# Kernel optimization log

Hardware: AMD Instinct MI355X
Metric: run time of the kernel (lower is better)

## Reference

```python
import jax, jax.numpy as jnp
import numpy as np

D_MODEL = 1024
N_HEADS = 16
D_K = D_MODEL // N_HEADS


def setup_inputs() -> dict:
    key = jax.random.key(0)
    ks = jax.random.split(key, 7)
    B, L = 1, 4096
    query = jax.random.normal(ks[0], (B, L, D_MODEL), dtype=jnp.float32)
    key_t = jax.random.normal(ks[1], (B, L, D_MODEL), dtype=jnp.float32)
    value = jax.random.normal(ks[2], (B, L, D_MODEL), dtype=jnp.float32)
    scale = 1.0 / np.sqrt(D_MODEL)
    # nn.Linear weight W has shape [out, in]; y = x @ W.T
    w_q = jax.random.normal(ks[3], (D_MODEL, D_MODEL), dtype=jnp.float32) * scale
    w_k = jax.random.normal(ks[4], (D_MODEL, D_MODEL), dtype=jnp.float32) * scale
    w_v = jax.random.normal(ks[5], (D_MODEL, D_MODEL), dtype=jnp.float32) * scale
    w_o = jax.random.normal(ks[6], (D_MODEL, D_MODEL), dtype=jnp.float32) * scale
    return {"query": query, "key": key_t, "value": value,
            "w_q": w_q, "w_k": w_k, "w_v": w_v, "w_o": w_o}


def reference(query, key, value, w_q, w_k, w_v, w_o):
    B, L, _ = query.shape
    # projections (Linear: x @ W.T)
    Q = (query @ w_q.T).reshape(B, L, N_HEADS, D_K).transpose(0, 2, 1, 3)
    K = (key @ w_k.T).reshape(B, L, N_HEADS, D_K).transpose(0, 2, 1, 3)
    V = (value @ w_v.T).reshape(B, L, N_HEADS, D_K).transpose(0, 2, 1, 3)
    # scaled dot-product attention with materialized [B,H,L,L] scores
    scores = jnp.einsum('bhqd,bhkd->bhqk', Q, K) / jnp.sqrt(jnp.float32(D_K))
    attn = jax.nn.softmax(scores, axis=-1)
    out = jnp.einsum('bhqk,bhkd->bhqd', attn, V)  # [B,H,L,d_k]
    out = out.transpose(0, 2, 1, 3).reshape(B, L, D_MODEL)
    return out @ w_o.T
```

## Files before the change

### kernel.cpp

```cpp
#include <hip/hip_runtime.h>
#include <hip/hip_bf16.h>
#include <hip/hip_fp16.h>
#include <cstdint>
#include <math.h>

#define DMODEL 1024
#define SEQ    4096
#define NHEAD  16
#define DK     64

typedef __attribute__((ext_vector_type(8))) short bf16x8;
typedef __attribute__((ext_vector_type(8))) _Float16 f16x8;
typedef __attribute__((ext_vector_type(4))) float f32x4;
typedef unsigned short u16;

__device__ __forceinline__ u16 f2bf(float f) {
    union { float f; unsigned int u; } v; v.f = f;
    unsigned int u = v.u;
    u += 0x7FFFu + ((u >> 16) & 1u);
    return (u16)(u >> 16);
}
__device__ __forceinline__ float bf2f(u16 h) {
    union { unsigned int u; float f; } v; v.u = ((unsigned int)h) << 16;
    return v.f;
}
__device__ __forceinline__ u16 f2h(float f) {
    __half h = __float2half_rn(f);
    union { __half h; u16 u; } v; v.h = h; return v.u;
}
__device__ __forceinline__ float h2f(u16 x) {
    union { u16 u; __half h; } v; v.u = x;
    return __half2float(v.h);
}
__device__ __forceinline__ unsigned int pk_bf16(float a, float b) {
    union { __hip_bfloat162 h; unsigned int u; } v;
    v.h = __float22bfloat162_rn(make_float2(a, b));
    return v.u;
}
__device__ __forceinline__ float fast_exp2(float x) {
    float r; asm("v_exp_f32 %0, %1" : "=v"(r) : "v"(x)); return r;
}

__global__ __launch_bounds__(256) void fallback_marker(float* __restrict__ out, int n) {
    int i = blockIdx.x * 256 + threadIdx.x;
    if (i < n) out[i] = (i == 0) ? 12345.0f : 0.0f;
}

__device__ __forceinline__ void split4_store(const float* __restrict__ in,
                                             u16* __restrict__ hi,
                                             u16* __restrict__ lo, int i) {
    float4 v = ((const float4*)in)[i];
    u16 h0 = f2h(v.x), h1 = f2h(v.y), h2 = f2h(v.z), h3 = f2h(v.w);
    ushort4 hv; hv.x = h0; hv.y = h1; hv.z = h2; hv.w = h3;
    ushort4 lv;
    lv.x = f2h(v.x - h2f(h0)); lv.y = f2h(v.y - h2f(h1));
    lv.z = f2h(v.z - h2f(h2)); lv.w = f2h(v.w - h2f(h3));
    ((ushort4*)hi)[i] = hv;
    ((ushort4*)lo)[i] = lv;
}

__global__ __launch_bounds__(256) void split_kernel(const float* __restrict__ in,
                                                    u16* __restrict__ hi,
                                                    u16* __restrict__ lo, int n4) {
    int i = blockIdx.x * 256 + threadIdx.x;
    if (i < n4) split4_store(in, hi, lo, i);
}

__global__ __launch_bounds__(256) void split_pair(const float* __restrict__ a_in,
                                                  u16* __restrict__ a_hi,
                                                  u16* __restrict__ a_lo, int a_n4,
                                                  const float* __restrict__ w_in,
                                                  u16* __restrict__ w_hi,
                                                  u16* __restrict__ w_lo, int w_n4) {
    int i = blockIdx.x * 256 + threadIdx.x;
    if (blockIdx.y == 0) {
        if (i < a_n4) split4_store(a_in, a_hi, a_lo, i);
    } else {
        if (i < w_n4) split4_store(w_in, w_hi, w_lo, i);
    }
}

__device__ __forceinline__ void gemm_core_fp16(const u16* __restrict__ aHi,
                                               const u16* __restrict__ aLo,
                                               const u16* __restrict__ bHi,
                                               int bm, int bn,
                                               f32x4 (&acc)[2][4]) {
    __shared__ u16 sAh[128 * 72], sAl[128 * 72];
    __shared__ u16 sBh[64 * 72];

    const int tid  = threadIdx.x;
    const int wave = tid >> 6;
    const int lane = tid & 63;
    const int quad = lane >> 4;
    const int l15  = lane & 15;
    const int srow = tid >> 2;
    const int scol = (tid & 3) * 16;

    const u16* pAh0 = aHi + (size_t)(bm + srow) * DMODEL + scol;
    const u16* pAh1 = aHi + (size_t)(bm + 64 + srow) * DMODEL + scol;
    const u16* pAl0 = aLo + (size_t)(bm + srow) * DMODEL + scol;
    const u16* pAl1 = aLo + (size_t)(bm + 64 + srow) * DMODEL + scol;
    const u16* pBh  = bHi + (size_t)(bn + srow) * DMODEL + scol;

    for (int k0 = 0; k0 < DMODEL; k0 += 64) {
        uint4 ah00 = *(const uint4*)(pAh0 + k0);
        uint4 ah01 = *(const uint4*)(pAh0 + k0 + 8);
        uint4 ah10 = *(const uint4*)(pAh1 + k0);
        uint4 ah11 = *(const uint4*)(pAh1 + k0 + 8);
        uint4 al00 = *(const uint4*)(pAl0 + k0);
        uint4 al01 = *(const uint4*)(pAl0 + k0 + 8);
        uint4 al10 = *(const uint4*)(pAl1 + k0);
        uint4 al11 = *(const uint4*)(pAl1 + k0 + 8);
        uint4 bh0  = *(const uint4*)(pBh + k0);
        uint4 bh1  = *(const uint4*)(pBh + k0 + 8);

        __syncthreads();
        *(uint4*)&sAh[srow * 72 + scol]            = ah00;
        *(uint4*)&sAh[srow * 72 + scol + 8]        = ah01;
        *(uint4*)&sAh[(64 + srow) * 72 + scol]     = ah10;
        *(uint4*)&sAh[(64 + srow) * 72 + scol + 8] = ah11;
        *(uint4*)&sAl[srow * 72 + scol]            = al00;
        *(uint4*)&sAl[srow * 72 + scol + 8]        = al01;
        *(uint4*)&sAl[(64 + srow) * 72 + scol]     = al10;
        *(uint4*)&sAl[(64 + srow) * 72 + scol + 8] = al11;
        *(uint4*)&sBh[srow * 72 + scol]            = bh0;
        *(uint4*)&sBh[srow * 72 + scol + 8]        = bh1;
        __syncthreads();

#pragma unroll
        for (int c = 0; c < 2; c++) {
            f16x8 ah[2], al[2];
#pragma unroll
            for (int m = 0; m < 2; m++) {
                const int aoff = (wave * 32 + m * 16 + l15) * 72 + c * 32 + quad * 8;
                ah[m] = *(const f16x8*)&sAh[aoff];
                al[m] = *(const f16x8*)&sAl[aoff];
            }
#pragma unroll
            for (int nt = 0; nt < 4; nt++) {
                const int boff = (nt * 16 + l15) * 72 + c * 32 + quad * 8;
                f16x8 bhf = *(const f16x8*)&sBh[boff];
#pragma unroll
                for (int m = 0; m < 2; m++) {
                    acc[m][nt] = __builtin_amdgcn_mfma_f32_16x16x32_f16(ah[m], bhf, acc[m][nt], 0, 0, 0);
                    acc[m][nt] = __builtin_amdgcn_mfma_f32_16x16x32_f16(al[m], bhf, acc[m][nt], 0, 0, 0);
                }
            }
        }
    }
}

__global__ __launch_bounds__(256) void proj_hl_bf(const u16* __restrict__ aHi,
                                                  const u16* __restrict__ aLo,
                                                  const u16* __restrict__ bHi,
                                                  u16* __restrict__ C,
                                                  int ldc, float scale) {
    const int bm = blockIdx.x * 128;
    const int bn = blockIdx.y * 64;
    f32x4 acc[2][4] = {};
    gemm_core_fp16(aHi, aLo, bHi, bm, bn, acc);
    const int lane = threadIdx.x & 63;
    const int wave = threadIdx.x >> 6;
    const int quad = lane >> 4;
    const int l15  = lane & 15;
#pragma unroll
    for (int m = 0; m < 2; m++)
#pragma unroll
        for (int nt = 0; nt < 4; nt++) {
            int col = bn + nt * 16 + l15;
#pragma unroll
            for (int r = 0; r < 4; r++) {
                int row = bm + wave * 32 + m * 16 + quad * 4 + r;
                C[(size_t)row * ldc + col] = f2bf(acc[m][nt][r] * scale);
            }
        }
}

__global__ __launch_bounds__(256) void proj_hl_f32(const u16* __restrict__ aHi,
                                                   const u16* __restrict__ aLo,
                                                   const u16* __restrict__ bHi,
                                                   float* __restrict__ C) {
    const int bm = blockIdx.x * 128;
    const int bn = blockIdx.y * 64;
    f32x4 acc[2][4] = {};
    gemm_core_fp16(aHi, aLo, bHi, bm, bn, acc);
    const int lane = threadIdx.x & 63;
    const int wave = threadIdx.x >> 6;
    const int quad = lane >> 4;
    const int l15  = lane & 15;
#pragma unroll
    for (int m = 0; m < 2; m++)
#pragma unroll
        for (int nt = 0; nt < 4; nt++) {
            int col = bn + nt * 16 + l15;
#pragma unroll
            for (int r = 0; r < 4; r++) {
                int row = bm + wave * 32 + m * 16 + quad * 4 + r;
                C[(size_t)row * DMODEL + col] = acc[m][nt][r];
            }
        }
}

#define PST 72

__global__ __launch_bounds__(256) void attn_mfma(const u16* __restrict__ Q,
                                                 const u16* __restrict__ K,
                                                 const u16* __restrict__ Vt,
                                                 u16* __restrict__ AOh,
                                                 u16* __restrict__ AOl) {
    __shared__ u16 sK[2][64 * 72];
    __shared__ u16 sV[2][64 * 72];
    __shared__ u16 sP[4 * 32 * PST];

    const int lin  = blockIdx.y * gridDim.x + blockIdx.x;
    const int swz  = (lin & 7) * 64 + (lin >> 3);
    const int head = swz >> 5;
    const int q0   = (swz & 31) * 128;

    const int tid  = threadIdx.x;
    const int wave = tid >> 6;
    const int lane = tid & 63;
    const int quad = lane >> 4;
    const int l15  = lane & 15;
    const int srow = tid >> 2;
    const int scol = (tid & 3) * 16;

    bf16x8 qf[2][2];
#pragma unroll
    for (int m = 0; m < 2; m++) {
        const u16* qb = Q + (size_t)(q0 + wave * 32 + m * 16 + l15) * DMODEL + head * DK;
        qf[m][0] = *(const bf16x8*)(qb + quad * 8);
        qf[m][1] = *(const bf16x8*)(qb + 32 + quad * 8);
    }

    f32x4 oacc[2][4] = {};
    float l_part[2] = {0.0f, 0.0f};

    const u16* Kst = K  + (size_t)srow * DMODEL + head * DK + scol;
    const u16* Vst = Vt + (size_t)(head * DK + srow) * SEQ + scol;
    u16* sPw = sP + wave * 32 * PST;

    {
        uint4 kv0 = *(const uint4*)(Kst);
        uint4 kv1 = *(const uint4*)(Kst + 8);
        uint4 vv0 = *(const uint4*)(Vst);
        uint4 vv1 = *(const uint4*)(Vst + 8);
        *(uint4*)&sK[0][srow * 72 + scol]     = kv0;
        *(uint4*)&sK[0][srow * 72 + scol + 8] = kv1;
        *(uint4*)&sV[0][srow * 72 + scol]     = vv0;
        *(uint4*)&sV[0][srow * 72 + scol + 8] = vv1;
    }
    __syncthreads();

    int cur = 0;
    for (int k0 = 0; k0 < SEQ; k0 += 64) {
        uint4 nkv0, nkv1, nvv0, nvv1;
        const bool has_next = (k0 + 64 < SEQ);
        if (has_next) {
            nkv0 = *(const uint4*)(Kst + (size_t)(k0 + 64) * DMODEL);
            nkv1 = *(const uint4*)(Kst + (size_t)(k0 + 64) * DMODEL + 8);
            nvv0 = *(const uint4*)(Vst + k0 + 64);
            nvv1 = *(const uint4*)(Vst + k0 + 64 + 8);
        }

        f32x4 s[4][2] = {};
#pragma unroll
        for (int nt = 0; nt < 4; nt++) {
            bf16x8 kf0 = *(const bf16x8*)&sK[cur][(nt * 16 + l15) * 72 + quad * 8];
            bf16x8 kf1 = *(const bf16x8*)&sK[cur][(nt * 16 + l15) * 72 + 32 + quad * 8];
#pragma unroll
            for (int m = 0; m < 2; m++) {
                s[nt][m] = __builtin_amdgcn_mfma_f32_16x16x32_bf16(kf0, qf[m][0], s[nt][m], 0, 0, 0);
                s[nt][m] = __builtin_amdgcn_mfma_f32_16x16x32_bf16(kf1, qf[m][1], s[nt][m], 0, 0, 0);
            }
        }

#pragma unroll
        for (int m = 0; m < 2; m++)
#pragma unroll
            for (int nt = 0; nt < 4; nt++) {
                float p0 = fast_exp2(s[nt][m][0]);
                float p1 = fast_exp2(s[nt][m][1]);
                float p2 = fast_exp2(s[nt][m][2]);
                float p3 = fast_exp2(s[nt][m][3]);
                l_part[m] += (p0 + p1) + (p2 + p3);
                uint2 w;
                w.x = pk_bf16(p0, p1);
                w.y = pk_bf16(p2, p3);
                *(uint2*)&sPw[(m * 16 + l15) * PST + nt * 16 + quad * 4] = w;
            }

#pragma unroll
        for (int c = 0; c < 2; c++) {
            bf16x8 pf0 = *(const bf16x8*)&sPw[(0 * 16 + l15) * PST + c * 32 + quad * 8];
            bf16x8 pf1 = *(const bf16x8*)&sPw[(1 * 16 + l15) * PST + c * 32 + quad * 8];
#pragma unroll
            for (int nt = 0; nt < 4; nt++) {
                bf16x8 vf = *(const bf16x8*)&sV[cur][(nt * 16 + l15) * 72 + c * 32 + quad * 8];
                oacc[0][nt] = __builtin_amdgcn_mfma_f32_16x16x32_bf16(pf0, vf, oacc[0][nt], 0, 0, 0);
                oacc[1][nt] = __builtin_amdgcn_mfma_f32_16x16x32_bf16(pf1, vf, oacc[1][nt], 0, 0, 0);
            }
        }

        if (has_next) {
            const int nxt = cur ^ 1;
            *(uint4*)&sK[nxt][srow * 72 + scol]     = nkv0;
            *(uint4*)&sK[nxt][srow * 72 + scol + 8] = nkv1;
            *(uint4*)&sV[nxt][srow * 72 + scol]     = nvv0;
            *(uint4*)&sV[nxt][srow * 72 + scol + 8] = nvv1;
        }
        __syncthreads();
        cur ^= 1;
    }

    float lf[2];
#pragma unroll
    for (int m = 0; m < 2; m++) {
        float l = l_part[m];
        l += __shfl_xor(l, 16);
        l += __shfl_xor(l, 32);
        lf[m] = l;
    }
#pragma unroll
    for (int m = 0; m < 2; m++) {
        float l_i[4];
#pragma unroll
        for (int r = 0; r < 4; r++)
            l_i[r] = __shfl(lf[m], (lane & 48) | (quad * 4 + r));
#pragma unroll
        for (int nt = 0; nt < 4; nt++) {
            int col = head * DK + nt * 16 + l15;
#pragma unroll
            for (int r = 0; r < 4; r++) {
                int row = q0 + wave * 32 + m * 16 + quad * 4 + r;
                float o = oacc[m][nt][r] / l_i[r];
                u16 h = f2h(o);
                AOh[(size_t)row * DMODEL + col] = h;
                AOl[(size_t)row * DMODEL + col] = f2h(o - h2f(h));
            }
        }
    }
}

extern "C" void kernel_launch(void* const* d_in, const int* in_sizes, int n_in,
                              void* d_out, int out_size, void* d_ws, size_t ws_size,
                              hipStream_t stream) {
    const float* query = (const float*)d_in[0];
    const float* key_t = (const float*)d_in[1];
    const float* value = (const float*)d_in[2];
    const float* wq    = (const float*)d_in[3];
    const float* wk    = (const float*)d_in[4];
    const float* wv    = (const float*)d_in[5];
    const float* wo    = (const float*)d_in[6];
    float* out = (float*)d_out;

    const size_t ACT_N = (size_t)SEQ * DMODEL;
    const size_t W_N   = (size_t)DMODEL * DMODEL;
    const size_t NEED  = 4 * ACT_N * sizeof(float);

    if (d_ws == nullptr || ws_size < NEED) {
        fallback_marker<<<dim3((out_size + 255) / 256), dim3(256), 0, stream>>>(out, out_size);
        return;
    }

    u16* ACT_HI = (u16*)d_ws;
    u16* ACT_LO = ACT_HI + ACT_N;
    u16* W_HI   = ACT_LO + ACT_N;
    u16* W_LO   = W_HI + W_N;
    u16* Qb     = W_LO + W_N;
    u16* Kb     = Qb + ACT_N;
    u16* Vt     = Kb + ACT_N;
    u16* AO_HI  = Vt + ACT_N;
    u16* AO_LO  = AO_HI + ACT_N;

    const int ACT4 = (int)(ACT_N / 4);
    const int W4   = (int)(W_N / 4);
    dim3 blk(256);
    dim3 pairg((ACT4 + 255) / 256, 2);
    dim3 wg((W4 + 255) / 256);

    const float QSCALE = 0.125f * 1.44269504f;

    split_pair<<<pairg, blk, 0, stream>>>(query, ACT_HI, ACT_LO, ACT4, wq, W_HI, W_LO, W4);
    proj_hl_bf<<<dim3(SEQ / 128, DMODEL / 64), blk, 0, stream>>>(
        ACT_HI, ACT_LO, W_HI, Qb, DMODEL, QSCALE);

    split_pair<<<pairg, blk, 0, stream>>>(key_t, ACT_HI, ACT_LO, ACT4, wk, W_HI, W_LO, W4);
    proj_hl_bf<<<dim3(SEQ / 128, DMODEL / 64), blk, 0, stream>>>(
        ACT_HI, ACT_LO, W_HI, Kb, DMODEL, 1.0f);

    split_pair<<<pairg, blk, 0, stream>>>(value, ACT_HI, ACT_LO, ACT4, wv, W_HI, W_LO, W4);
    proj_hl_bf<<<dim3(DMODEL / 128, SEQ / 64), blk, 0, stream>>>(
        W_HI, W_LO, ACT_HI, Vt, SEQ, 1.0f);

    attn_mfma<<<dim3(SEQ / 128, NHEAD), blk, 0, stream>>>(Qb, Kb, Vt, AO_HI, AO_LO);

    split_kernel<<<wg, blk, 0, stream>>>(wo, W_HI, W_LO, W4);
    proj_hl_f32<<<dim3(SEQ / 128, DMODEL / 64), blk, 0, stream>>>(
        AO_HI, AO_LO, W_HI, out);
}
```

Baseline: 334.9 us.

## Batch Q/K/V conversion and projections into single launches, drop lo-split term

Replaces the three split+projection pairs with one conversion kernel over all six inputs and one projection kernel covering the Q, K and V GEMMs, using a swizzled block index. The Q/K/V projections drop the fp16 low-residual term for activations, halving MFMA work and shared-memory traffic there. The output projection's weight split now writes only the high part. This cuts launch count and arithmetic, but lowers projection precision to plain fp16 inputs, which may affect accuracy.

```diff
diff --git a/kernel.cpp b/kernel.cpp
--- a/kernel.cpp
+++ b/kernel.cpp
@@ -46,38 +46,140 @@
     if (i < n) out[i] = (i == 0) ? 12345.0f : 0.0f;
 }
 
-__device__ __forceinline__ void split4_store(const float* __restrict__ in,
-                                             u16* __restrict__ hi,
-                                             u16* __restrict__ lo, int i) {
-    float4 v = ((const float4*)in)[i];
-    u16 h0 = f2h(v.x), h1 = f2h(v.y), h2 = f2h(v.z), h3 = f2h(v.w);
-    ushort4 hv; hv.x = h0; hv.y = h1; hv.z = h2; hv.w = h3;
-    ushort4 lv;
-    lv.x = f2h(v.x - h2f(h0)); lv.y = f2h(v.y - h2f(h1));
-    lv.z = f2h(v.z - h2f(h2)); lv.w = f2h(v.w - h2f(h3));
-    ((ushort4*)hi)[i] = hv;
-    ((ushort4*)lo)[i] = lv;
-}
-
-__global__ __launch_bounds__(256) void split_kernel(const float* __restrict__ in,
-                                                    u16* __restrict__ hi,
-                                                    u16* __restrict__ lo, int n4) {
+__global__ __launch_bounds__(256) void split_all(const float* __restrict__ q,
+                                                 const float* __restrict__ k,
+                                                 const float* __restrict__ v,
+                                                 const float* __restrict__ wq,
+                                                 const float* __restrict__ wk,
+                                                 const float* __restrict__ wv,
+                                                 u16* __restrict__ qh,
+                                                 u16* __restrict__ kh,
+                                                 u16* __restrict__ vh,
+                                                 u16* __restrict__ wqh,
+                                                 u16* __restrict__ wkh,
+                                                 u16* __restrict__ wvh,
+                                                 int act_n4, int w_n4) {
     int i = blockIdx.x * 256 + threadIdx.x;
-    if (i < n4) split4_store(in, hi, lo, i);
-}
-
-__global__ __launch_bounds__(256) void split_pair(const float* __restrict__ a_in,
-                                                  u16* __restrict__ a_hi,
-                                                  u16* __restrict__ a_lo, int a_n4,
-                                                  const float* __restrict__ w_in,
-                                                  u16* __restrict__ w_hi,
-                                                  u16* __restrict__ w_lo, int w_n4) {
+    const float* src; u16* dst; int n4;
+    switch (blockIdx.y) {
+        case 0:  src = q;  dst = qh;  n4 = act_n4; break;
+        case 1:  src = k;  dst = kh;  n4 = act_n4; break;
+        case 2:  src = v;  dst = vh;  n4 = act_n4; break;
+        case 3:  src = wq; dst = wqh; n4 = w_n4;   break;
+        case 4:  src = wk; dst = wkh; n4 = w_n4;   break;
+        default: src = wv; dst = wvh; n4 = w_n4;   break;
+    }
+    if (i < n4) {
+        float4 f = ((const float4*)src)[i];
+        ushort4 h; h.x = f2h(f.x); h.y = f2h(f.y); h.z = f2h(f.z); h.w = f2h(f.w);
+        ((ushort4*)dst)[i] = h;
+    }
+}
+
+__global__ __launch_bounds__(256) void split_hi(const float* __restrict__ in,
+                                                u16* __restrict__ hi, int n4) {
     int i = blockIdx.x * 256 + threadIdx.x;
-    if (blockIdx.y == 0) {
-        if (i < a_n4) split4_store(a_in, a_hi, a_lo, i);
-    } else {
-        if (i < w_n4) split4_store(w_in, w_hi, w_lo, i);
-    }
+    if (i < n4) {
+        float4 f = ((const float4*)in)[i];
+        ushort4 h; h.x = f2h(f.x); h.y = f2h(f.y); h.z = f2h(f.z); h.w = f2h(f.w);
+        ((ushort4*)hi)[i] = h;
+    }
+}
+
+__device__ __forceinline__ void gemm_core_f16_1t(const u16* __restrict__ aHi,
+                                                 const u16* __restrict__ bHi,
+                                                 int bm, int bn,
+                                                 f32x4 (&acc)[2][4]) {
+    __shared__ u16 sAh[128 * 72];
+    __shared__ u16 sBh[64 * 72];
+
+    const int tid  = threadIdx.x;
+    const int wave = tid >> 6;
+    const int lane = tid & 63;
+    const int quad = lane >> 4;
+    const int l15  = lane & 15;
+    const int srow = tid >> 2;
+    const int scol = (tid & 3) * 16;
+
+    const u16* pA0 = aHi + (size_t)(bm + srow) * DMODEL + scol;
+    const u16* pA1 = aHi + (size_t)(bm + 64 + srow) * DMODEL + scol;
+    const u16* pB  = bHi + (size_t)(bn + srow) * DMODEL + scol;
+
+    for (int k0 = 0; k0 < DMODEL; k0 += 64) {
+        uint4 a00 = *(const uint4*)(pA0 + k0);
+        uint4 a01 = *(const uint4*)(pA0 + k0 + 8);
+        uint4 a10 = *(const uint4*)(pA1 + k0);
+        uint4 a11 = *(const uint4*)(pA1 + k0 + 8);
+        uint4 b0  = *(const uint4*)(pB + k0);
+        uint4 b1  = *(const uint4*)(pB + k0 + 8);
+
+        __syncthreads();
+        *(uint4*)&sAh[srow * 72 + scol]            = a00;
+        *(uint4*)&sAh[srow * 72 + scol + 8]        = a01;
+        *(uint4*)&sAh[(64 + srow) * 72 + scol]     = a10;
+        *(uint4*)&sAh[(64 + srow) * 72 + scol + 8] = a11;
+        *(uint4*)&sBh[srow * 72 + scol]            = b0;
+        *(uint4*)&sBh[srow * 72 + scol + 8]        = b1;
+        __syncthreads();
+
+#pragma unroll
+        for (int c = 0; c < 2; c++) {
+            f16x8 ah[2];
+#pragma unroll
+            for (int m = 0; m < 2; m++) {
+                const int aoff = (wave * 32 + m * 16 + l15) * 72 + c * 32 + quad * 8;
+                ah[m] = *(const f16x8*)&sAh[aoff];
+            }
+#pragma unroll
+            for (int nt = 0; nt < 4; nt++) {
+                const int boff = (nt * 16 + l15) * 72 + c * 32 + quad * 8;
+                f16x8 bhf = *(const f16x8*)&sBh[boff];
+#pragma unroll
+                for (int m = 0; m < 2; m++)
+                    acc[m][nt] = __builtin_amdgcn_mfma_f32_16x16x32_f16(ah[m], bhf, acc[m][nt], 0, 0, 0);
+            }
+        }
+    }
+}
+
+__global__ __launch_bounds__(256) void proj_qkv(const u16* __restrict__ qh,
+                                                const u16* __restrict__ kh,
+                                                const u16* __restrict__ vh,
+                                                const u16* __restrict__ wqh,
+                                                const u16* __restrict__ wkh,
+                                                const u16* __restrict__ wvh,
+                                                u16* __restrict__ Qb,
+                                                u16* __restrict__ Kb,
+                                                u16* __restrict__ Vt,
+                                                float qscale) {
+    const int lin = blockIdx.y * gridDim.x + blockIdx.x;
+    const int swz = (lin & 7) * 192 + (lin >> 3);
+    const int z   = swz >> 9;
+    const int bx  = swz & 511;
+
+    const u16 *A, *B; u16* C; int bm, bn, ldc; float scale;
+    if (z == 0)      { A = qh;  B = wqh; C = Qb; bm = (bx & 31) * 128; bn = (bx >> 5) * 64; ldc = DMODEL; scale = qscale; }
+    else if (z == 1) { A = kh;  B = wkh; C = Kb; bm = (bx & 31) * 128; bn = (bx >> 5) * 64; ldc = DMODEL; scale = 1.0f; }
+    else             { A = wvh; B = vh;  C = Vt; bm = (bx & 7) * 128;  bn = (bx >> 3) * 64; ldc = SEQ;    scale = 1.0f; }
+
+    f32x4 acc[2][4] = {};
+    gemm_core_f16_1t(A, B, bm, bn, acc);
+
+    const int lane = threadIdx.x & 63;
+    const int wave = threadIdx.x >> 6;
+    const int quad = lane >> 4;
+    const int l15  = lane & 15;
+#pragma unroll
+    for (int m = 0; m < 2; m++)
+#pragma unroll
+        for (int nt = 0; nt < 4; nt++) {
+            int col = bn + nt * 16 + l15;
+#pragma unroll
+            for (int r = 0; r < 4; r++) {
+                int row = bm + wave * 32 + m * 16 + quad * 4 + r;
+                C[(size_t)row * ldc + col] = f2bf(acc[m][nt][r] * scale);
+            }
+        }
 }
 
 __device__ __forceinline__ void gemm_core_fp16(const u16* __restrict__ aHi,
@@ -150,32 +252,6 @@
     }
 }
 
-__global__ __launch_bounds__(256) void proj_hl_bf(const u16* __restrict__ aHi,
-                                                  const u16* __restrict__ aLo,
-                                                  const u16* __restrict__ bHi,
-                                                  u16* __restrict__ C,
-                                                  int ldc, float scale) {
-    const int bm = blockIdx.x * 128;
-    const int bn = blockIdx.y * 64;
-    f32x4 acc[2][4] = {};
-    gemm_core_fp16(aHi, aLo, bHi, bm, bn, acc);
-    const int lane = threadIdx.x & 63;
-    const int wave = threadIdx.x >> 6;
-    const int quad = lane >> 4;
-    const int l15  = lane & 15;
-#pragma unroll
-    for (int m = 0; m < 2; m++)
-#pragma unroll
-        for (int nt = 0; nt < 4; nt++) {
-            int col = bn + nt * 16 + l15;
-#pragma unroll
-            for (int r = 0; r < 4; r++) {
-                int row = bm + wave * 32 + m * 16 + quad * 4 + r;
-                C[(size_t)row * ldc + col] = f2bf(acc[m][nt][r] * scale);
-            }
-        }
-}
-
 __global__ __launch_bounds__(256) void proj_hl_f32(const u16* __restrict__ aHi,
                                                    const u16* __restrict__ aLo,
                                                    const u16* __restrict__ bHi,
@@ -363,39 +439,33 @@
         return;
     }
 
-    u16* ACT_HI = (u16*)d_ws;
-    u16* ACT_LO = ACT_HI + ACT_N;
-    u16* W_HI   = ACT_LO + ACT_N;
-    u16* W_LO   = W_HI + W_N;
-    u16* Qb     = W_LO + W_N;
-    u16* Kb     = Qb + ACT_N;
-    u16* Vt     = Kb + ACT_N;
-    u16* AO_HI  = Vt + ACT_N;
-    u16* AO_LO  = AO_HI + ACT_N;
+    u16* ACT0 = (u16*)d_ws;
+    u16* ACT1 = ACT0 + ACT_N;
+    u16* ACT2 = ACT1 + ACT_N;
+    u16* W0   = ACT2 + ACT_N;
+    u16* W1   = W0 + W_N;
+    u16* W2   = W1 + W_N;
+    u16* Qb   = W2 + W_N;
+    u16* Kb   = Qb + ACT_N;
+    u16* Vt   = Kb + ACT_N;
 
     const int ACT4 = (int)(ACT_N / 4);
     const int W4   = (int)(W_N / 4);
     dim3 blk(256);
-    dim3 pairg((ACT4 + 255) / 256, 2);
-    dim3 wg((W4 + 255) / 256);
 
     const float QSCALE = 0.125f * 1.44269504f;
 
-    split_pair<<<pairg, blk, 0, stream>>>(query, ACT_HI, ACT_LO, ACT4, wq, W_HI, W_LO, W4);
-    proj_hl_bf<<<dim3(SEQ / 128, DMODEL / 64), blk, 0, stream>>>(
-        ACT_HI, ACT_LO, W_HI, Qb, DMODEL, QSCALE);
-
-    split_pair<<<pairg, blk, 0, stream>>>(key_t, ACT_HI, ACT_LO, ACT4, wk, W_HI, W_LO, W4);
-    proj_hl_bf<<<dim3(SEQ / 128, DMODEL / 64), blk, 0, stream>>>(
-        ACT_HI, ACT_LO, W_HI, Kb, DMODEL, 1.0f);
-
-    split_pair<<<pairg, blk, 0, stream>>>(value, ACT_HI, ACT_LO, ACT4, wv, W_HI, W_LO, W4);
-    proj_hl_bf<<<dim3(DMODEL / 128, SEQ / 64), blk, 0, stream>>>(
-        W_HI, W_LO, ACT_HI, Vt, SEQ, 1.0f);
-
-    attn_mfma<<<dim3(SEQ / 128, NHEAD), blk, 0, stream>>>(Qb, Kb, Vt, AO_HI, AO_LO);
-
-    split_kernel<<<wg, blk, 0, stream>>>(wo, W_HI, W_LO, W4);
+    split_all<<<dim3((ACT4 + 255) / 256, 6), blk, 0, stream>>>(
+        query, key_t, value, wq, wk, wv,
+        ACT0, ACT1, ACT2, W0, W1, W2, ACT4, W4);
+
+    proj_qkv<<<dim3(512, 3), blk, 0, stream>>>(
+        ACT0, ACT1, ACT2, W0, W1, W2, Qb, Kb, Vt, QSCALE);
+
+    attn_mfma<<<dim3(SEQ / 128, NHEAD), blk, 0, stream>>>(Qb, Kb, Vt, ACT0, ACT1);
+
+    split_hi<<<dim3((W4 + 255) / 256), blk, 0, stream>>>(wo, W0, W4);
+
     proj_hl_f32<<<dim3(SEQ / 128, DMODEL / 64), blk, 0, stream>>>(
-        AO_HI, AO_LO, W_HI, out);
-}
+        ACT0, ACT1, W0, out);
+}
```

New measurement: 291.7 us. 1.15x faster.
